# Optimization experiments

Hardware: AMD Instinct MI355X
Metric: run time of the kernel (lower is better)

## Reference

```python
import jax, jax.numpy as jnp
import numpy as np

B, S, D_MODEL, D_ATTN = 4, 2048, 1024, 1024
NEG_INF = jnp.float32(-jnp.inf)


def setup_inputs() -> dict:
    key = jax.random.key(0)
    ks = jax.random.split(key, 6)
    scale = 1.0 / np.sqrt(D_MODEL)
    return {
        "x": jax.random.normal(ks[0], (B, S, D_MODEL), dtype=jnp.float32),
        "mask": jnp.ones((B, S), dtype=jnp.float32),
        "Wq": jax.random.normal(ks[1], (D_ATTN, D_MODEL), dtype=jnp.float32) * scale,
        "Wk": jax.random.normal(ks[2], (D_ATTN, D_MODEL), dtype=jnp.float32) * scale,
        "Wv": jax.random.normal(ks[3], (D_ATTN, D_MODEL), dtype=jnp.float32) * scale,
        "Wo": jax.random.normal(ks[4], (D_MODEL, D_ATTN), dtype=jnp.float32) * scale,
        "bo": jnp.zeros((D_MODEL,), dtype=jnp.float32),
    }


def reference(x, mask, Wq, Wk, Wv, Wo, bo):
    # x: [B,S,Dm]; torch Linear weight is [out,in], so y = x @ W.T
    q = jnp.einsum("bsd,ad->bsa", x, Wq)  # [B,S,Da]
    k = jnp.einsum("bsd,ad->bsa", x, Wk)
    v = jnp.einsum("bsd,ad->bsa", x, Wv)  # NOTE: v from x (original quirk)
    logits = jnp.einsum("bqa,bka->bqk", q, k)  # [B,S,S]
    # causal mask (cross_attention=True path): keep lower triangle incl. diag
    causal = jnp.tril(jnp.ones((S, S), dtype=bool))
    logits = jnp.where(causal[None], logits, NEG_INF)
    # padding mask: outer product of per-token mask
    square_mask = mask[:, :, None] * mask[:, None, :]  # [B,S,S]
    logits = jnp.where(square_mask == 1, logits, NEG_INF)
    # scale by sqrt(d_model) AFTER masking (as in original)
    attn = jax.nn.softmax(logits / jnp.sqrt(jnp.float32(D_MODEL)), axis=-1)
    attn_out = jnp.einsum("bqk,bka->bqa", attn, v)  # [B,S,Da]
    return jnp.einsum("bsa,da->bsd", attn_out, Wo) + bo
```

## Files before the change

kernel.cpp:

```cpp
#include <hip/hip_runtime.h>
#include <hip/hip_bf16.h>
#include <cstdio>

typedef __bf16 bf16x8 __attribute__((ext_vector_type(8)));
typedef float f32x4 __attribute__((ext_vector_type(4)));

#define BM 128
#define BN 128
#define BK 64

__device__ __forceinline__ unsigned short f2bf(float f) {
  union { float f; unsigned u; } v; v.f = f;
  unsigned u = v.u;
  return (unsigned short)((u + 0x7FFFu + ((u >> 16) & 1u)) >> 16);
}

__device__ __forceinline__ float bf2f(unsigned short s) {
  union { unsigned u; float f; } v; v.u = ((unsigned)s) << 16;
  return v.f;
}

#define GLOAD16(gsrc, ldst) \
  __builtin_amdgcn_global_load_lds((const __attribute__((address_space(1))) void*)(gsrc), \
                                   (__attribute__((address_space(3))) void*)(ldst), 16, 0, 0)

template<int EPI>
__global__ __launch_bounds__(256, 2)
void gemm_bt(const unsigned short* __restrict__ A, const unsigned short* __restrict__ B,
             void* __restrict__ Cv, void* __restrict__ Cv2, const float* __restrict__ bias,
             int K, int ldA, int ldB, int ldC,
             long aBat, long bBat, long cBat,
             int causalSkip, int causalKlim, float scale, int revM)
{
  const int by = revM ? (gridDim.y - 1 - blockIdx.y) : blockIdx.y;
  const int m0 = by * BM;
  const int n0 = blockIdx.x * BN;
  if (causalSkip && n0 > m0) return;
  const int bz = blockIdx.z;

  const unsigned short* Ab = A + (long)bz * aBat + (long)m0 * ldA;
  const unsigned short* Bb = B + (long)bz * bBat + (long)n0 * ldB;

  __shared__ short lds[2][2][BM * BK];

  const int tid = threadIdx.x;
  const int lane = tid & 63;
  const int wave = tid >> 6;
  const int wr = wave >> 1, wc = wave & 1;

  const int Keff = causalKlim ? min(K, m0 + BM) : K;
  const int nk = Keff / BK;

  const int srow = tid >> 3;
  const int sch = tid & 7;

  const f32x4 fzero = {0.f, 0.f, 0.f, 0.f};
  f32x4 acc[4][4];
#pragma unroll
  for (int i = 0; i < 4; i++)
#pragma unroll
    for (int j = 0; j < 4; j++) acc[i][j] = fzero;

  int aOff[4][2], bOff[4][2];
#pragma unroll
  for (int i = 0; i < 4; i++) {
#pragma unroll
    for (int s = 0; s < 2; s++) {
      int ra = wr * 64 + i * 16 + (lane & 15);
      aOff[i][s] = ra * BK + (((s * 4 + (lane >> 4)) ^ (ra & 7)) * 8);
      int rb = wc * 64 + i * 16 + (lane & 15);
      bOff[i][s] = rb * BK + (((s * 4 + (lane >> 4)) ^ (rb & 7)) * 8);
    }
  }

  auto stage = [&](int buf, int kt) {
    const unsigned short* Ak = Ab + kt * BK;
    const unsigned short* Bk = Bb + kt * BK;
#pragma unroll
    for (int r = 0; r < 4; r++) {
      int row = r * 32 + srow;
      int sc = sch ^ (row & 7);
      GLOAD16(Ak + (long)row * ldA + sc * 8, &lds[buf][0][(r * 32 + wave * 8) * BK]);
    }
#pragma unroll
    for (int r = 0; r < 4; r++) {
      int row = r * 32 + srow;
      int sc = sch ^ (row & 7);
      GLOAD16(Bk + (long)row * ldB + sc * 8, &lds[buf][1][(r * 32 + wave * 8) * BK]);
    }
  };

  stage(0, 0);
  __syncthreads();

  int cur = 0;
  for (int kt = 0; kt < nk; kt++) {
    if (kt + 1 < nk) stage(cur ^ 1, kt + 1);
    const short* La = lds[cur][0];
    const short* Lb = lds[cur][1];
#pragma unroll
    for (int s = 0; s < 2; s++) {
      bf16x8 av[4], bv[4];
#pragma unroll
      for (int i = 0; i < 4; i++) av[i] = *reinterpret_cast<const bf16x8*>(La + aOff[i][s]);
#pragma unroll
      for (int j = 0; j < 4; j++) bv[j] = *reinterpret_cast<const bf16x8*>(Lb + bOff[j][s]);
#pragma unroll
      for (int i = 0; i < 4; i++)
#pragma unroll
        for (int j = 0; j < 4; j++)
          acc[i][j] = __builtin_amdgcn_mfma_f32_16x16x32_bf16(av[i], bv[j], acc[i][j], 0, 0, 0);
    }
    __syncthreads();
    cur ^= 1;
  }

  const int rb4 = (lane >> 4) * 4;
  const int cl = lane & 15;
#pragma unroll
  for (int i = 0; i < 4; i++) {
#pragma unroll
    for (int j = 0; j < 4; j++) {
      const int gm = m0 + wr * 64 + i * 16 + rb4;
      const int gn = n0 + wc * 64 + j * 16 + cl;
      if (EPI == 0) {
        unsigned short* C = (unsigned short*)Cv + (long)bz * cBat;
#pragma unroll
        for (int r = 0; r < 4; r++)
          C[(long)(gm + r) * ldC + gn] = f2bf(acc[i][j][r] * scale);
      } else if (EPI == 2) {
        float* C = (float*)Cv;
        const float bb = bias[gn];
#pragma unroll
        for (int r = 0; r < 4; r++)
          C[(long)(gm + r) * ldC + gn] = acc[i][j][r] + bb;
      } else if (EPI == 4) {
        if (gn < 2048) {
          unsigned short* C = (unsigned short*)Cv;
#pragma unroll
          for (int r = 0; r < 4; r++)
            C[(long)(gm + r) * ldC + gn] = f2bf(acc[i][j][r]);
        } else {
          const int d = gn - 2048;
          const int b = gm >> 11;
          const int sIdx = gm & 2047;
          unsigned short* C = (unsigned short*)Cv2 + (long)b * (2048L * 1024)
                              + (long)d * 2048 + sIdx;
          ushort4 pk;
          pk.x = f2bf(acc[i][j][0]);
          pk.y = f2bf(acc[i][j][1]);
          pk.z = f2bf(acc[i][j][2]);
          pk.w = f2bf(acc[i][j][3]);
          *reinterpret_cast<ushort4*>(C) = pk;
        }
      }
    }
  }
}

__global__ __launch_bounds__(256)
void softmax_rows(const unsigned short* __restrict__ Sb, const float* __restrict__ maskv,
                  unsigned short* __restrict__ P, int Sdim)
{
  const int q = blockIdx.x;
  const int b = blockIdx.y;
  const int kmax = (q & ~127) + 128;
  const unsigned short* row = Sb + ((long)b * Sdim + q) * Sdim;
  unsigned short* prow = P + ((long)b * Sdim + q) * Sdim;
  const float* mrow = maskv + (long)b * Sdim;
  const int tid = threadIdx.x;
  const float mq = mrow[q];
  const int k0 = tid * 8;
  const bool live = (k0 < kmax);

  float v[8];
  if (live) {
    uint4 raw = *reinterpret_cast<const uint4*>(row + k0);
    const unsigned short* us = reinterpret_cast<const unsigned short*>(&raw);
    float4 ma = *reinterpret_cast<const float4*>(mrow + k0);
    float4 mb = *reinterpret_cast<const float4*>(mrow + k0 + 4);
    float mv[8] = {ma.x, ma.y, ma.z, ma.w, mb.x, mb.y, mb.z, mb.w};
#pragma unroll
    for (int u = 0; u < 8; u++) {
      const int k = k0 + u;
      const bool ok = (k <= q) && (mq * mv[u] == 1.0f);
      v[u] = ok ? bf2f(us[u]) : -INFINITY;
    }
  } else {
#pragma unroll
    for (int u = 0; u < 8; u++) v[u] = -INFINITY;
  }

  float mx = -INFINITY;
#pragma unroll
  for (int u = 0; u < 8; u++) mx = fmaxf(mx, v[u]);
#pragma unroll
  for (int o = 32; o; o >>= 1) mx = fmaxf(mx, __shfl_xor(mx, o));
  __shared__ float redm[4], reds[4];
  if ((tid & 63) == 0) redm[tid >> 6] = mx;
  __syncthreads();
  mx = fmaxf(fmaxf(redm[0], redm[1]), fmaxf(redm[2], redm[3]));

  float p[8];
  float sm = 0.f;
#pragma unroll
  for (int u = 0; u < 8; u++) {
    p[u] = (v[u] > -INFINITY) ? __expf(v[u] - mx) : 0.f;
    sm += p[u];
  }
#pragma unroll
  for (int o = 32; o; o >>= 1) sm += __shfl_xor(sm, o);
  if ((tid & 63) == 0) reds[tid >> 6] = sm;
  __syncthreads();
  sm = reds[0] + reds[1] + reds[2] + reds[3];
  const float inv = 1.0f / sm;

  if (live) {
    union { unsigned short us[8]; uint4 u4; } pk;
#pragma unroll
    for (int u = 0; u < 8; u++) pk.us[u] = f2bf(p[u] * inv);
    *reinterpret_cast<uint4*>(prow + k0) = pk.u4;
  }
}

__global__ __launch_bounds__(256)
void cast_f32_bf16(const float* __restrict__ in, unsigned short* __restrict__ out, int n)
{
  const int i = (blockIdx.x * 256 + threadIdx.x) * 8;
  if (i >= n) return;
  float4 a = *reinterpret_cast<const float4*>(in + i);
  float4 b = *reinterpret_cast<const float4*>(in + i + 4);
  union { unsigned short us[8]; uint4 u4; } pk;
  pk.us[0] = f2bf(a.x); pk.us[1] = f2bf(a.y); pk.us[2] = f2bf(a.z); pk.us[3] = f2bf(a.w);
  pk.us[4] = f2bf(b.x); pk.us[5] = f2bf(b.y); pk.us[6] = f2bf(b.z); pk.us[7] = f2bf(b.w);
  *reinterpret_cast<uint4*>(out + i) = pk.u4;
}

__global__ __launch_bounds__(256)
void cast_weights(const float* __restrict__ w0, const float* __restrict__ w1,
                  const float* __restrict__ w2, const float* __restrict__ w3,
                  unsigned short* __restrict__ dqkv, unsigned short* __restrict__ dout)
{
  const int z = blockIdx.z;
  const float* src = (z == 0) ? w0 : (z == 1) ? w1 : (z == 2) ? w2 : w3;
  unsigned short* dst = (z < 3) ? (dqkv + (long)z * 1024 * 1024) : dout;
  const int i = (blockIdx.x * 256 + threadIdx.x) * 8;
  float4 a = *reinterpret_cast<const float4*>(src + i);
  float4 b = *reinterpret_cast<const float4*>(src + i + 4);
  union { unsigned short us[8]; uint4 u4; } pk;
  pk.us[0] = f2bf(a.x); pk.us[1] = f2bf(a.y); pk.us[2] = f2bf(a.z); pk.us[3] = f2bf(a.w);
  pk.us[4] = f2bf(b.x); pk.us[5] = f2bf(b.y); pk.us[6] = f2bf(b.z); pk.us[7] = f2bf(b.w);
  *reinterpret_cast<uint4*>(dst + i) = pk.u4;
}

extern "C" void kernel_launch(void* const* d_in, const int* in_sizes, int n_in,
                              void* d_out, int out_size, void* d_ws, size_t ws_size,
                              hipStream_t stream)
{
  const int B = 4, S = 2048, D = 1024;
  const float* x  = (const float*)d_in[0];
  const float* mk = (const float*)d_in[1];
  const float* Wq = (const float*)d_in[2];
  const float* Wk = (const float*)d_in[3];
  const float* Wv = (const float*)d_in[4];
  const float* Wo = (const float*)d_in[5];
  const float* bo = (const float*)d_in[6];
  float* out = (float*)d_out;

  char* ws = (char*)d_ws;
  const long MB = 1024L * 1024L;
  unsigned short* Xbf  = (unsigned short*)(ws + 0);
  unsigned short* QKb  = (unsigned short*)(ws + 16 * MB);
  unsigned short* Vt   = (unsigned short*)(ws + 48 * MB);
  unsigned short* Wqkv = (unsigned short*)(ws + 64 * MB);
  unsigned short* Wob  = (unsigned short*)(ws + 70 * MB);
  unsigned short* Sbuf = (unsigned short*)(ws + 72 * MB);
  unsigned short* P    = QKb;
  unsigned short* O    = Xbf;

  if (ws_size < (size_t)(104 * MB)) {
    fprintf(stderr, "kernel_launch: ws too small (%zu bytes, need 104MB)\n", ws_size);
    return;
  }

  cast_f32_bf16<<<dim3((B * S * D) / 8 / 256), 256, 0, stream>>>(x, Xbf, B * S * D);
  cast_weights<<<dim3((D * D) / 8 / 256, 1, 4), 256, 0, stream>>>(Wq, Wk, Wv, Wo, Wqkv, Wob);

  const dim3 blk(256);
  dim3 gQKV(3072 / BN, 8192 / BM, 1);
  gemm_bt<4><<<gQKV, blk, 0, stream>>>(Xbf, Wqkv, QKb, Vt, nullptr,
                                       1024, 1024, 1024, 2048,
                                       0, 0, 0, 0, 0, 1.0f, 0);
  dim3 gS(2048 / BN, 2048 / BM, 4);
  gemm_bt<0><<<gS, blk, 0, stream>>>(QKb, QKb + 1024, Sbuf, nullptr, nullptr,
                                     1024, 2048, 2048, 2048,
                                     (long)S * 2048, (long)S * 2048, (long)S * S,
                                     1, 0, 0.03125f, 0);
  softmax_rows<<<dim3(2048, 4), blk, 0, stream>>>(Sbuf, mk, P, 2048);
  dim3 gO(1024 / BN, 2048 / BM, 4);
  gemm_bt<0><<<gO, blk, 0, stream>>>(P, Vt, O, nullptr, nullptr,
                                     2048, 2048, 2048, 1024,
                                     (long)S * S, (long)D * S, (long)S * D,
                                     0, 1, 1.0f, 1);
  dim3 gF(1024 / BN, 8192 / BM, 1);
  gemm_bt<2><<<gF, blk, 0, stream>>>(O, Wob, out, nullptr, bo,
                                     1024, 1024, 1024, 1024,
                                     0, 0, 0, 0, 0, 1.0f, 0);
}
```

Before: 185.9 us.

## Deepen GEMM prefetch to two tiles ahead and add XCD-aware block swizzle

```diff
diff --git a/kernel.cpp b/kernel.cpp
--- a/kernel.cpp
+++ b/kernel.cpp
@@ -32,9 +32,18 @@
              long aBat, long bBat, long cBat,
              int causalSkip, int causalKlim, float scale, int revM)
 {
-  const int by = revM ? (gridDim.y - 1 - blockIdx.y) : blockIdx.y;
+  const int gx = gridDim.x;
+  const int nwg = gx * gridDim.y;
+  const int flat = blockIdx.y * gx + blockIdx.x;
+  const int qch = nwg >> 3, rch = nwg & 7;
+  const int xcd = flat & 7, idx = flat >> 3;
+  const int swz = (xcd < rch ? xcd * (qch + 1) : rch * (qch + 1) + (xcd - rch) * qch) + idx;
+  const int bx = swz % gx;
+  int by = swz / gx;
+  if (revM) by = gridDim.y - 1 - by;
+
   const int m0 = by * BM;
-  const int n0 = blockIdx.x * BN;
+  const int n0 = bx * BN;
   if (causalSkip && n0 > m0) return;
   const int bz = blockIdx.z;
 
@@ -91,27 +100,50 @@
   };
 
   stage(0, 0);
-  __syncthreads();
+  stage(1, 1);
+  asm volatile("s_waitcnt vmcnt(8)" ::: "memory");
+  __builtin_amdgcn_sched_barrier(0);
+  __builtin_amdgcn_s_barrier();
 
   int cur = 0;
   for (int kt = 0; kt < nk; kt++) {
-    if (kt + 1 < nk) stage(cur ^ 1, kt + 1);
     const short* La = lds[cur][0];
     const short* Lb = lds[cur][1];
+    bf16x8 av[2][4], bv[2][4];
 #pragma unroll
     for (int s = 0; s < 2; s++) {
-      bf16x8 av[4], bv[4];
-#pragma unroll
-      for (int i = 0; i < 4; i++) av[i] = *reinterpret_cast<const bf16x8*>(La + aOff[i][s]);
-#pragma unroll
-      for (int j = 0; j < 4; j++) bv[j] = *reinterpret_cast<const bf16x8*>(Lb + bOff[j][s]);
+#pragma unroll
+      for (int i = 0; i < 4; i++) {
+        av[s][i] = *reinterpret_cast<const bf16x8*>(La + aOff[i][s]);
+        bv[s][i] = *reinterpret_cast<const bf16x8*>(Lb + bOff[i][s]);
+      }
+    }
+    asm volatile("s_waitcnt lgkmcnt(0)" ::: "memory");
+    __builtin_amdgcn_sched_barrier(0);
+    __builtin_amdgcn_s_barrier();
+    __builtin_amdgcn_sched_barrier(0);
+
+    if (kt + 2 < nk) {
+      stage(cur, kt + 2);
+      asm volatile("s_waitcnt vmcnt(8)" ::: "memory");
+    } else if (kt + 1 < nk) {
+      asm volatile("s_waitcnt vmcnt(0)" ::: "memory");
+    }
+    if (kt + 1 < nk) {
+      __builtin_amdgcn_s_barrier();
+      __builtin_amdgcn_sched_barrier(0);
+    }
+
+    __builtin_amdgcn_s_setprio(1);
+#pragma unroll
+    for (int s = 0; s < 2; s++)
 #pragma unroll
       for (int i = 0; i < 4; i++)
 #pragma unroll
         for (int j = 0; j < 4; j++)
-          acc[i][j] = __builtin_amdgcn_mfma_f32_16x16x32_bf16(av[i], bv[j], acc[i][j], 0, 0, 0);
-    }
-    __syncthreads();
+          acc[i][j] = __builtin_amdgcn_mfma_f32_16x16x32_bf16(av[s][i], bv[s][j], acc[i][j], 0, 0, 0);
+    __builtin_amdgcn_s_setprio(0);
+    __builtin_amdgcn_sched_barrier(0);
     cur ^= 1;
   }
 
```

Measured after the change: 180.7 us. 1.03x faster.
